# Performance work log

Measured on AMD Instinct MI355X. Metric: run time of the kernel, lower is better.

Reference implementation:

```python
import jax, jax.numpy as jnp
import numpy as np

HIDDEN = 4096
N_HEADS = 32
N_KV_HEADS = 8
HEAD_DIM = 128
ROPE_THETA = 10000.0
B, S = 2, 2048


def _rope_cos_sin(seq_len, head_dim, theta):
    inv_freq = 1.0 / (theta ** (jnp.arange(0, head_dim, 2, dtype=jnp.float32) / head_dim))
    t = jnp.arange(seq_len, dtype=jnp.float32)
    freqs = jnp.einsum('i,j->ij', t, inv_freq)          # [S, D/2]
    emb = jnp.concatenate([freqs, freqs], axis=-1)      # [S, D]
    return jnp.cos(emb), jnp.sin(emb)


def _rotate_half(x):
    x1, x2 = x[..., : x.shape[-1] // 2], x[..., x.shape[-1] // 2 :]
    return jnp.concatenate([-x2, x1], axis=-1)


def setup_inputs() -> dict:
    key = jax.random.key(0)
    k0, k1, k2, k3, k4 = jax.random.split(key, 5)
    scale = 0.02
    return {
        'hidden_states': jax.random.normal(k0, (B, S, HIDDEN), dtype=jnp.float32),
        'wq': jax.random.normal(k1, (N_HEADS * HEAD_DIM, HIDDEN), dtype=jnp.float32) * scale,
        'wk': jax.random.normal(k2, (N_KV_HEADS * HEAD_DIM, HIDDEN), dtype=jnp.float32) * scale,
        'wv': jax.random.normal(k3, (N_KV_HEADS * HEAD_DIM, HIDDEN), dtype=jnp.float32) * scale,
        'wo': jax.random.normal(k4, (HIDDEN, N_HEADS * HEAD_DIM), dtype=jnp.float32) * scale,
    }


def reference(hidden_states, wq, wk, wv, wo):
    bsz, q_len, _ = hidden_states.shape
    n_rep = N_HEADS // N_KV_HEADS

    # Q/K/V projections (nn.Linear: x @ W.T), reshape to [B, H, S, D]
    q = (hidden_states @ wq.T).reshape(bsz, q_len, N_HEADS, HEAD_DIM).transpose(0, 2, 1, 3)
    k = (hidden_states @ wk.T).reshape(bsz, q_len, N_KV_HEADS, HEAD_DIM).transpose(0, 2, 1, 3)
    v = (hidden_states @ wv.T).reshape(bsz, q_len, N_KV_HEADS, HEAD_DIM).transpose(0, 2, 1, 3)

    # RoPE (position_ids = arange) broadcast over heads: cos/sin [1,1,S,D]
    cos, sin = _rope_cos_sin(q_len, HEAD_DIM, ROPE_THETA)
    cos = cos[None, None]
    sin = sin[None, None]
    q = q * cos + _rotate_half(q) * sin
    k = k * cos + _rotate_half(k) * sin

    # repeat_kv: [B, KVH, S, D] -> [B, H, S, D]
    k = jnp.repeat(k, n_rep, axis=1)
    v = jnp.repeat(v, n_rep, axis=1)

    # scaled dot-product attention with causal mask
    scores = jnp.einsum('bhqd,bhkd->bhqk', q, k) / jnp.sqrt(jnp.float32(HEAD_DIM))
    causal = jnp.tril(jnp.ones((q_len, q_len), dtype=bool))
    scores = jnp.where(causal[None, None], scores, jnp.finfo(scores.dtype).min)
    probs = jax.nn.softmax(scores.astype(jnp.float32), axis=-1).astype(q.dtype)
    attn = jnp.einsum('bhqk,bhkd->bhqd', probs, v)

    # merge heads and output projection
    attn = attn.transpose(0, 2, 1, 3).reshape(bsz, q_len, N_HEADS * HEAD_DIM)
    return attn @ wo.T
```

## Files before the change

### kernel.cpp

```cpp
#include <hip/hip_runtime.h>
#include <hip/hip_bf16.h>

typedef __attribute__((ext_vector_type(8))) __bf16 bf16x8;
typedef __attribute__((ext_vector_type(4))) float f32x4;

#define SEQ 2048
#define BATCH 2
#define LDQ 6144

__device__ __forceinline__ void stc(float* p, float v)          { *p = v; }
__device__ __forceinline__ void stc(__hip_bfloat16* p, float v) { *p = __float2bfloat16(v); }

__device__ __forceinline__ void async_copy16(const __hip_bfloat16* g, __hip_bfloat16* lds) {
    __builtin_amdgcn_global_load_lds(
        (const __attribute__((address_space(1))) unsigned int*)g,
        (__attribute__((address_space(3))) unsigned int*)lds,
        16, 0, 0);
}

__global__ void f2b_kernel(const float* __restrict__ s, __hip_bfloat16* __restrict__ d, int n8)
{
    const int i = blockIdx.x * blockDim.x + threadIdx.x;
    if (i >= n8) return;
    const float4 a = ((const float4*)s)[i * 2];
    const float4 b = ((const float4*)s)[i * 2 + 1];
    __hip_bfloat16 t[8];
    t[0] = __float2bfloat16(a.x); t[1] = __float2bfloat16(a.y);
    t[2] = __float2bfloat16(a.z); t[3] = __float2bfloat16(a.w);
    t[4] = __float2bfloat16(b.x); t[5] = __float2bfloat16(b.y);
    t[6] = __float2bfloat16(b.z); t[7] = __float2bfloat16(b.w);
    ((uint4*)d)[i] = *(const uint4*)t;
}

template<typename TC>
__global__ __launch_bounds__(256) void gemm_bt_kernel(
    const __hip_bfloat16* __restrict__ A,
    const __hip_bfloat16* __restrict__ B,
    TC* __restrict__ C,
    int M, int N, int K)
{
    __shared__ __align__(16) __hip_bfloat16 As[128][32];
    __shared__ __align__(16) __hip_bfloat16 Bs[128][32];

    const int tid  = threadIdx.x;
    const int wave = tid >> 6;
    const int lane = tid & 63;
    const int quad = lane >> 4;
    const int l16  = lane & 15;
    const int m0 = blockIdx.x * 128;
    const int n0 = blockIdx.y * 128;
    const int wr = (wave >> 1) * 64;
    const int wc = (wave & 1) * 64;

    const int ch0   = wave * 128;
    const int lrow  = lane >> 2;
    const int lcol8 = (lane & 3) * 8;

    f32x4 acc[4][4] = {};

    for (int k0 = 0; k0 < K; k0 += 32) {
        __syncthreads();
        for (int j = 0; j < 2; j++) {
            const int row = (ch0 >> 2) + j * 16 + lrow;
            async_copy16(A + (size_t)(m0 + row) * K + k0 + lcol8,
                         &As[0][0] + (ch0 + j * 64) * 8);
            async_copy16(B + (size_t)(n0 + row) * K + k0 + lcol8,
                         &Bs[0][0] + (ch0 + j * 64) * 8);
        }
        __syncthreads();

        bf16x8 af[4], bf[4];
        for (int i = 0; i < 4; i++) {
            af[i] = *(const bf16x8*)(&As[wr + i * 16 + l16][quad * 8]);
            bf[i] = *(const bf16x8*)(&Bs[wc + i * 16 + l16][quad * 8]);
        }
        for (int i = 0; i < 4; i++)
            for (int j = 0; j < 4; j++)
                acc[i][j] = __builtin_amdgcn_mfma_f32_16x16x32_bf16(af[i], bf[j], acc[i][j], 0, 0, 0);
    }

    for (int i = 0; i < 4; i++)
        for (int j = 0; j < 4; j++)
            for (int r = 0; r < 4; r++) {
                const int m = m0 + wr + i * 16 + quad * 4 + r;
                const int n = n0 + wc + j * 16 + l16;
                stc(&C[(size_t)m * N + n], acc[i][j][r]);
            }
}

__global__ void rope_kernel(__hip_bfloat16* __restrict__ X, int rows, int n_heads,
                            int ld, int col0)
{
    const int idx = blockIdx.x * blockDim.x + threadIdx.x;
    const int total = rows * n_heads * 64;
    if (idx >= total) return;
    const int j   = idx & 63;
    const int h   = (idx >> 6) % n_heads;
    const int row = idx / (n_heads * 64);
    const int s   = row & (SEQ - 1);

    const float invf = expf(-(float)j * (9.210340371976184f / 64.0f));
    const float ang = (float)s * invf;
    const float c = cosf(ang), sn = sinf(ang);

    const size_t base = (size_t)row * ld + col0 + h * 128;
    const float x1 = __bfloat162float(X[base + j]);
    const float x2 = __bfloat162float(X[base + 64 + j]);
    X[base + j]      = __float2bfloat16(x1 * c - x2 * sn);
    X[base + 64 + j] = __float2bfloat16(x2 * c + x1 * sn);
}

__global__ __launch_bounds__(256) void vtrans_kernel(
    const __hip_bfloat16* __restrict__ V, __hip_bfloat16* __restrict__ VT)
{
    __shared__ unsigned int T[64][65];

    const int tid = threadIdx.x;
    const int n0 = blockIdx.x * 64;
    const int s0 = blockIdx.y * 64;
    const int b  = blockIdx.z;

    #pragma unroll
    for (int it = 0; it < 2; it++) {
        const int idx = it * 256 + tid;
        const int sr = idx >> 3, nc = (idx & 7) * 8;
        const uint4 v = *(const uint4*)(V + (size_t)(b * SEQ + s0 + sr) * LDQ + n0 + nc);
        const unsigned short* u = (const unsigned short*)&v;
        #pragma unroll
        for (int i = 0; i < 8; i++) T[sr][nc + i] = u[i];
    }
    __syncthreads();
    #pragma unroll
    for (int it = 0; it < 2; it++) {
        const int idx = it * 256 + tid;
        const int nn = idx >> 3, sc = (idx & 7) * 8;
        unsigned short u[8];
        #pragma unroll
        for (int i = 0; i < 8; i++) u[i] = (unsigned short)T[sc + i][nn];
        *(uint4*)(VT + (size_t)(b * 1024 + n0 + nn) * SEQ + s0 + sc) = *(const uint4*)u;
    }
}

__global__ __launch_bounds__(64) void attn_kernel(
    const __hip_bfloat16* __restrict__ QKV,
    const __hip_bfloat16* __restrict__ VT,
    __hip_bfloat16* __restrict__ O)
{
    __shared__ __align__(16) __hip_bfloat16 Pw[2][16][72];

    const int lane = threadIdx.x;
    const int quad = lane >> 4;
    const int l16  = lane & 15;
    const int h   = blockIdx.y;
    const int b   = blockIdx.z;
    const int kvh = h >> 2;

    bf16x8 ones;
    {
        __hip_bfloat16 t[8];
        for (int i = 0; i < 8; i++) t[i] = __float2bfloat16(1.0f);
        ones = *(const bf16x8*)t;
    }

    const __hip_bfloat16* Kbase = QKV + (size_t)b * SEQ * LDQ + 4096 + kvh * 128 + quad * 8;
    const __hip_bfloat16* Vbase = VT + (size_t)(b * 1024 + kvh * 128) * SEQ + quad * 8;
    const float scale = 0.08838834764831845f;
    const float shift = 12.0f;

    for (int ph = 0; ph < 2; ph++) {
        const int qt = ph ? blockIdx.x : 63 - blockIdx.x;
        const int q0 = qt * 32;

        bf16x8 aq[2][4];
        for (int ch = 0; ch < 2; ch++)
            for (int c = 0; c < 4; c++)
                aq[ch][c] = *(const bf16x8*)(QKV + (size_t)(b * SEQ + q0 + ch * 16 + l16) * LDQ
                                                 + h * 128 + c * 32 + quad * 8);

        f32x4 o[2][8] = {};
        f32x4 lsum[2] = {};

        const int nt = qt / 2 + 1;
        for (int kt = 0; kt < nt; kt++) {
            f32x4 sc[2][4] = {};
            #pragma unroll
            for (int g = 0; g < 4; g++) {
                const __hip_bfloat16* kr = Kbase + (size_t)(kt * 64 + g * 16 + l16) * LDQ;
                bf16x8 bk[4];
                #pragma unroll
                for (int c = 0; c < 4; c++) bk[c] = *(const bf16x8*)(kr + c * 32);
                #pragma unroll
                for (int c = 0; c < 4; c++) {
                    sc[0][g] = __builtin_amdgcn_mfma_f32_16x16x32_bf16(aq[0][c], bk[c], sc[0][g], 0, 0, 0);
                    sc[1][g] = __builtin_amdgcn_mfma_f32_16x16x32_bf16(aq[1][c], bk[c], sc[1][g], 0, 0, 0);
                }
            }

            const bool diag = (kt == nt - 1);
            #pragma unroll
            for (int ch = 0; ch < 2; ch++)
                #pragma unroll
                for (int rr = 0; rr < 4; rr++) {
                    float s[4];
                    #pragma unroll
                    for (int g = 0; g < 4; g++) s[g] = sc[ch][g][rr] * scale - shift;
                    if (diag) {
                        const int qg = q0 + ch * 16 + quad * 4 + rr;
                        #pragma unroll
                        for (int g = 0; g < 4; g++)
                            if (kt * 64 + g * 16 + l16 > qg) s[g] = -1e30f;
                    }
                    #pragma unroll
                    for (int g = 0; g < 4; g++)
                        Pw[ch][quad * 4 + rr][g * 16 + l16] = __float2bfloat16(__expf(s[g]));
                }
            asm volatile("s_waitcnt lgkmcnt(0)" ::: "memory");

            bf16x8 ap[2][2];
            #pragma unroll
            for (int ch = 0; ch < 2; ch++) {
                ap[ch][0] = *(const bf16x8*)(&Pw[ch][l16][quad * 8]);
                ap[ch][1] = *(const bf16x8*)(&Pw[ch][l16][32 + quad * 8]);
                lsum[ch] = __builtin_amdgcn_mfma_f32_16x16x32_bf16(ap[ch][0], ones, lsum[ch], 0, 0, 0);
                lsum[ch] = __builtin_amdgcn_mfma_f32_16x16x32_bf16(ap[ch][1], ones, lsum[ch], 0, 0, 0);
            }

            #pragma unroll
            for (int nc = 0; nc < 8; nc++) {
                const __hip_bfloat16* vr = Vbase + (size_t)(nc * 16 + l16) * SEQ + kt * 64;
                const bf16x8 bv0 = *(const bf16x8*)(vr);
                const bf16x8 bv1 = *(const bf16x8*)(vr + 32);
                o[0][nc] = __builtin_amdgcn_mfma_f32_16x16x32_bf16(ap[0][0], bv0, o[0][nc], 0, 0, 0);
                o[0][nc] = __builtin_amdgcn_mfma_f32_16x16x32_bf16(ap[0][1], bv1, o[0][nc], 0, 0, 0);
                o[1][nc] = __builtin_amdgcn_mfma_f32_16x16x32_bf16(ap[1][0], bv0, o[1][nc], 0, 0, 0);
                o[1][nc] = __builtin_amdgcn_mfma_f32_16x16x32_bf16(ap[1][1], bv1, o[1][nc], 0, 0, 0);
            }
        }

        for (int ch = 0; ch < 2; ch++)
            for (int rr = 0; rr < 4; rr++) {
                const float inv = 1.0f / lsum[ch][rr];
                const size_t row = (size_t)(b * SEQ + q0 + ch * 16 + quad * 4 + rr);
                for (int nc = 0; nc < 8; nc++)
                    O[row * 4096 + h * 128 + nc * 16 + l16] = __float2bfloat16(o[ch][nc][rr] * inv);
            }
    }
}

extern "C" void kernel_launch(void* const* d_in, const int* in_sizes, int n_in,
                              void* d_out, int out_size, void* d_ws, size_t ws_size,
                              hipStream_t stream)
{
    const float* X  = (const float*)d_in[0];
    const float* Wq = (const float*)d_in[1];
    const float* Wk = (const float*)d_in[2];
    const float* Wv = (const float*)d_in[3];
    const float* Wo = (const float*)d_in[4];
    float* out = (float*)d_out;

    const size_t MB = 1048576;
    char* ws = (char*)d_ws;
    __hip_bfloat16* Xb   = (__hip_bfloat16*)(ws);
    __hip_bfloat16* WB   = (__hip_bfloat16*)(ws + 32 * MB);
    __hip_bfloat16* Wkb  = (__hip_bfloat16*)(ws + 64 * MB);
    __hip_bfloat16* Wvb  = (__hip_bfloat16*)(ws + 72 * MB);
    __hip_bfloat16* QKVb = (__hip_bfloat16*)(ws + 80 * MB);
    __hip_bfloat16* Ab   = Xb;
    __hip_bfloat16* Wob  = WB;
    __hip_bfloat16* VT   = Wkb;

    const int M = BATCH * SEQ;

    f2b_kernel<<<(M * 4096 / 8 + 255) / 256, 256, 0, stream>>>(X,  Xb,  M * 4096 / 8);
    f2b_kernel<<<(4096 * 4096 / 8 + 255) / 256, 256, 0, stream>>>(Wq, WB,  4096 * 4096 / 8);
    f2b_kernel<<<(1024 * 4096 / 8 + 255) / 256, 256, 0, stream>>>(Wk, Wkb, 1024 * 4096 / 8);
    f2b_kernel<<<(1024 * 4096 / 8 + 255) / 256, 256, 0, stream>>>(Wv, Wvb, 1024 * 4096 / 8);

    gemm_bt_kernel<__hip_bfloat16>
        <<<dim3(M / 128, LDQ / 128), 256, 0, stream>>>(Xb, WB, QKVb, M, LDQ, 4096);

    f2b_kernel<<<(4096 * 4096 / 8 + 255) / 256, 256, 0, stream>>>(Wo, Wob, 4096 * 4096 / 8);

    rope_kernel<<<(M * 32 * 64 + 255) / 256, 256, 0, stream>>>(QKVb, M, 32, LDQ, 0);
    rope_kernel<<<(M * 8 * 64 + 255) / 256, 256, 0, stream>>>(QKVb, M, 8, LDQ, 4096);

    vtrans_kernel<<<dim3(16, SEQ / 64, BATCH), 256, 0, stream>>>(QKVb + 5120, VT);

    attn_kernel<<<dim3(32, 32, BATCH), 64, 0, stream>>>(QKVb, VT, Ab);

    gemm_bt_kernel<float>
        <<<dim3(M / 128, 4096 / 128), 256, 0, stream>>>(Ab, Wob, out, M, 4096, 4096);
}
```

Before: 932.9 us.

## Replace GEMM with 256x256 double-buffered pipelined kernel and XCD-aware tile mapping

Replaces the 128x128 single-buffered GEMM with a 256x256-tile, 512-thread kernel. It prefetches K-tiles asynchronously into double-buffered LDS, interleaved with MFMA phases. Workgroup IDs are remapped so neighbouring tiles land on the same XCD, and s_setprio is raised around MFMA bursts. The goal is to hide global load latency and raise data reuse, at the cost of higher register and LDS pressure, possible spills, and fewer workgroups per GEMM.

```diff
diff --git a/kernel.cpp b/kernel.cpp
--- a/kernel.cpp
+++ b/kernel.cpp
@@ -33,57 +33,106 @@
 }
 
 template<typename TC>
-__global__ __launch_bounds__(256) void gemm_bt_kernel(
+__global__ __launch_bounds__(512, 2) void gemm256_kernel(
     const __hip_bfloat16* __restrict__ A,
     const __hip_bfloat16* __restrict__ B,
     TC* __restrict__ C,
     int M, int N, int K)
 {
-    __shared__ __align__(16) __hip_bfloat16 As[128][32];
-    __shared__ __align__(16) __hip_bfloat16 Bs[128][32];
+    __shared__ __align__(16) __hip_bfloat16 sAB[2][2][2][256][32];
+    const int NT = K >> 6;
 
     const int tid  = threadIdx.x;
     const int wave = tid >> 6;
     const int lane = tid & 63;
     const int quad = lane >> 4;
     const int l16  = lane & 15;
-    const int m0 = blockIdx.x * 128;
-    const int n0 = blockIdx.y * 128;
-    const int wr = (wave >> 1) * 64;
-    const int wc = (wave & 1) * 64;
-
-    const int ch0   = wave * 128;
-    const int lrow  = lane >> 2;
-    const int lcol8 = (lane & 3) * 8;
-
-    f32x4 acc[4][4] = {};
-
-    for (int k0 = 0; k0 < K; k0 += 32) {
-        __syncthreads();
-        for (int j = 0; j < 2; j++) {
-            const int row = (ch0 >> 2) + j * 16 + lrow;
-            async_copy16(A + (size_t)(m0 + row) * K + k0 + lcol8,
-                         &As[0][0] + (ch0 + j * 64) * 8);
-            async_copy16(B + (size_t)(n0 + row) * K + k0 + lcol8,
-                         &Bs[0][0] + (ch0 + j * 64) * 8);
+    const int wm = wave >> 2;
+    const int wn = wave & 3;
+
+    const int nbm = M >> 8;
+    const int nwg = nbm * (N >> 8);
+    int wg = blockIdx.x;
+    {
+        const int q8 = nwg >> 3, r8 = nwg & 7;
+        const int xcd = wg & 7, base = wg >> 3;
+        wg = (xcd < r8 ? xcd * (q8 + 1) : r8 * (q8 + 1) + (xcd - r8) * q8) + base;
+    }
+    const int m0 = (wg % nbm) << 8;
+    const int n0 = (wg / nbm) << 8;
+
+    const int srow = lane >> 2;
+    const int scol = (lane & 3) * 8;
+
+    auto stage = [&](int tile, int matr, int kh) {
+        const __hip_bfloat16* g = matr ? B : A;
+        const int b0 = matr ? n0 : m0;
+        const int buf = tile & 1;
+        #pragma unroll
+        for (int j = 0; j < 2; ++j) {
+            const int c = wave * 2 + j;
+            async_copy16(g + (size_t)(b0 + c * 16 + srow) * K + tile * 64 + kh * 32 + scol,
+                         &sAB[buf][matr][kh][c * 16][0]);
         }
-        __syncthreads();
-
-        bf16x8 af[4], bf[4];
-        for (int i = 0; i < 4; i++) {
-            af[i] = *(const bf16x8*)(&As[wr + i * 16 + l16][quad * 8]);
-            bf[i] = *(const bf16x8*)(&Bs[wc + i * 16 + l16][quad * 8]);
+    };
+
+    stage(0, 0, 0); stage(0, 1, 0); stage(0, 0, 1); stage(0, 1, 1);
+    stage(1, 0, 0); stage(1, 1, 0);
+    asm volatile("s_waitcnt vmcnt(4)" ::: "memory");
+    __builtin_amdgcn_s_barrier();
+
+    f32x4 acc[8][4] = {};
+    bf16x8 bv[4];
+
+    for (int T = 0; T < NT; ++T) {
+        const int buf = T & 1;
+        #pragma unroll
+        for (int q = 0; q < 4; ++q) {
+            const int kh = q >> 1;
+            const int rh = (q == 1 || q == 2) ? 1 : 0;
+
+            bf16x8 av[4];
+            #pragma unroll
+            for (int i = 0; i < 4; ++i)
+                av[i] = *(const bf16x8*)&sAB[buf][0][kh][wm * 128 + (rh * 4 + i) * 16 + l16][quad * 8];
+            if (q == 0 || q == 2) {
+                #pragma unroll
+                for (int j = 0; j < 4; ++j)
+                    bv[j] = *(const bf16x8*)&sAB[buf][1][kh][wn * 64 + j * 16 + l16][quad * 8];
+            }
+
+            if (q == 0) { if (T + 1 < NT) stage(T + 1, 0, 1); }
+            if (q == 1) { if (T + 1 < NT) stage(T + 1, 1, 1); }
+            if (q == 2) { if (T + 2 < NT) stage(T + 2, 0, 0); }
+            if (q == 3) { if (T + 2 < NT) stage(T + 2, 1, 0); }
+
+            __builtin_amdgcn_s_barrier();
+            asm volatile("s_waitcnt lgkmcnt(0)" ::: "memory");
+            __builtin_amdgcn_s_setprio(1);
+            #pragma unroll
+            for (int i = 0; i < 4; ++i)
+                #pragma unroll
+                for (int j = 0; j < 4; ++j)
+                    acc[rh * 4 + i][j] = __builtin_amdgcn_mfma_f32_16x16x32_bf16(
+                        av[i], bv[j], acc[rh * 4 + i][j], 0, 0, 0);
+            __builtin_amdgcn_s_setprio(0);
+
+            if (q == 3) {
+                if (T < NT - 2)       asm volatile("s_waitcnt vmcnt(4)" ::: "memory");
+                else if (T == NT - 2) asm volatile("s_waitcnt vmcnt(0)" ::: "memory");
+            }
+            __builtin_amdgcn_s_barrier();
         }
-        for (int i = 0; i < 4; i++)
-            for (int j = 0; j < 4; j++)
-                acc[i][j] = __builtin_amdgcn_mfma_f32_16x16x32_bf16(af[i], bf[j], acc[i][j], 0, 0, 0);
-    }
-
-    for (int i = 0; i < 4; i++)
-        for (int j = 0; j < 4; j++)
-            for (int r = 0; r < 4; r++) {
-                const int m = m0 + wr + i * 16 + quad * 4 + r;
-                const int n = n0 + wc + j * 16 + l16;
+    }
+
+    #pragma unroll
+    for (int i = 0; i < 8; ++i)
+        #pragma unroll
+        for (int j = 0; j < 4; ++j)
+            #pragma unroll
+            for (int r = 0; r < 4; ++r) {
+                const int m = m0 + wm * 128 + i * 16 + quad * 4 + r;
+                const int n = n0 + wn * 64 + j * 16 + l16;
                 stc(&C[(size_t)m * N + n], acc[i][j][r]);
             }
 }
@@ -276,8 +325,8 @@
     f2b_kernel<<<(1024 * 4096 / 8 + 255) / 256, 256, 0, stream>>>(Wk, Wkb, 1024 * 4096 / 8);
     f2b_kernel<<<(1024 * 4096 / 8 + 255) / 256, 256, 0, stream>>>(Wv, Wvb, 1024 * 4096 / 8);
 
-    gemm_bt_kernel<__hip_bfloat16>
-        <<<dim3(M / 128, LDQ / 128), 256, 0, stream>>>(Xb, WB, QKVb, M, LDQ, 4096);
+    gemm256_kernel<__hip_bfloat16>
+        <<<dim3((M / 256) * (LDQ / 256)), 512, 0, stream>>>(Xb, WB, QKVb, M, LDQ, 4096);
 
     f2b_kernel<<<(4096 * 4096 / 8 + 255) / 256, 256, 0, stream>>>(Wo, Wob, 4096 * 4096 / 8);
 
@@ -288,6 +337,6 @@
 
     attn_kernel<<<dim3(32, 32, BATCH), 64, 0, stream>>>(QKVb, VT, Ab);
 
-    gemm_bt_kernel<float>
-        <<<dim3(M / 128, 4096 / 128), 256, 0, stream>>>(Ab, Wob, out, M, 4096, 4096);
-}
+    gemm256_kernel<float>
+        <<<dim3((M / 256) * (4096 / 256)), 512, 0, stream>>>(Ab, Wob, out, M, 4096, 4096);
+}
```

Measured after the change: 872.1 us. 1.07x faster.
